# Performance work log

Hardware: AMD Instinct MI355X
Metric: run time of the kernel (lower is better)

Reference implementation:

```python
import jax, jax.numpy as jnp
import numpy as np

NUM_NODES = 50000
NUM_EDGES = 800000
DIM = 96


def setup_inputs() -> dict:
    key = jax.random.key(0)
    k1, k2, k3, k4, k5, k6 = jax.random.split(key, 6)
    x = jax.random.normal(k1, (NUM_NODES, DIM), dtype=jnp.float32)
    edge_index = jax.random.randint(k2, (2, NUM_EDGES), 0, NUM_NODES, dtype=jnp.int64)
    s = 1.0 / np.sqrt(DIM)
    W_self = jax.random.uniform(k3, (DIM, DIM), dtype=jnp.float32, minval=-s, maxval=s)
    b_self = jax.random.uniform(k4, (DIM,), dtype=jnp.float32, minval=-s, maxval=s)
    W_neigh = jax.random.uniform(k5, (DIM, DIM), dtype=jnp.float32, minval=-s, maxval=s)
    b_neigh = jax.random.uniform(k6, (DIM,), dtype=jnp.float32, minval=-s, maxval=s)
    return {"x": x, "edge_index": edge_index, "W_self": W_self, "b_self": b_self,
            "W_neigh": W_neigh, "b_neigh": b_neigh}


def reference(x, edge_index, W_self, b_self, W_neigh, b_neigh):
    source, target = edge_index[0], edge_index[1]
    # scatter-add of gathered source features into target rows
    aggregated = jax.ops.segment_sum(x[source], target, num_segments=NUM_NODES)  # [N, D]
    degree = jax.ops.segment_sum(jnp.ones((NUM_EDGES,), dtype=x.dtype), target,
                                 num_segments=NUM_NODES)[:, None]  # [N, 1]
    neighbor_mean = aggregated / jnp.maximum(degree, 1.0)
    # nn.Linear applies x @ W.T + b
    return x @ W_self.T + b_self + neighbor_mean @ W_neigh.T + b_neigh
```

## Files before the change

### kernel.cpp

```cpp
#include <hip/hip_runtime.h>
#include <hip/hip_bf16.h>

#define N_NODES 50000
#define N_EDGES 800000
#define DIM 96
#define NPART 256
#define PSZ 196
#define NBINBLK 196
#define BINCAP 48
#define BPP (NBINBLK * BINCAP)
#define CAP 4096
#define NPACK_BLOCKS 4688

typedef unsigned int uint;
typedef unsigned short u16;
using u16x8 = __attribute__((ext_vector_type(8))) unsigned short;

__device__ __forceinline__ u16 f2bf(float f) {
    __hip_bfloat16 h = __float2bfloat16(f);
    return *reinterpret_cast<u16*>(&h);
}
__device__ __forceinline__ float bf2f(u16 u) {
    return __uint_as_float(((uint)u) << 16);
}
__device__ __forceinline__ int pdiv(int t) { return (int)(((uint)t * 85599u) >> 24); }

__global__ __launch_bounds__(256) void packbin_k(
    const float* __restrict__ x, const int* __restrict__ ei,
    u16* __restrict__ xbf, uint* __restrict__ part_edges,
    int* __restrict__ counts)
{
    __shared__ uint bins[NPART * BINCAP];
    __shared__ int  bcnt[NPART];
    const int tid = threadIdx.x;

    if (blockIdx.x >= NBINBLK) {
        int pb = blockIdx.x - NBINBLK;
        int i4 = (pb * 256 + tid) * 4;
        if (i4 < N_NODES * DIM) {
            float4 v = *reinterpret_cast<const float4*>(x + i4);
            ushort4 o;
            o.x = f2bf(v.x); o.y = f2bf(v.y); o.z = f2bf(v.z); o.w = f2bf(v.w);
            *reinterpret_cast<ushort4*>(xbf + i4) = o;
        }
        return;
    }

    for (int i = tid; i < NPART; i += 256) bcnt[i] = 0;
    __syncthreads();

    const int e0 = blockIdx.x * 4096 + tid * 16;
    if (e0 + 16 <= N_EDGES) {
#pragma unroll
        for (int j = 0; j < 4; j++) {
            int4 s = *reinterpret_cast<const int4*>(ei + e0 + j * 4);
            int4 t = *reinterpret_cast<const int4*>(ei + N_EDGES + e0 + j * 4);
            int ss[4] = {s.x, s.y, s.z, s.w};
            int tt[4] = {t.x, t.y, t.z, t.w};
#pragma unroll
            for (int k = 0; k < 4; k++) {
                int p = pdiv(tt[k]);
                int local = tt[k] - p * PSZ;
                int slot = atomicAdd(&bcnt[p], 1);
                if (slot < BINCAP)
                    bins[p * BINCAP + slot] = ((uint)local << 16) | (uint)ss[k];
            }
        }
    } else {
        for (int j = 0; j < 16; j++) {
            int e = e0 + j;
            if (e < N_EDGES) {
                int sv = ei[e];
                int tv = ei[N_EDGES + e];
                int p = pdiv(tv);
                int local = tv - p * PSZ;
                int slot = atomicAdd(&bcnt[p], 1);
                if (slot < BINCAP)
                    bins[p * BINCAP + slot] = ((uint)local << 16) | (uint)sv;
            }
        }
    }
    __syncthreads();

    for (int p = tid; p < NPART; p += 256)
        counts[p * NBINBLK + blockIdx.x] = min(bcnt[p], BINCAP);

    for (int i = tid; i < NPART * BINCAP; i += 256) {
        int p = i / BINCAP;
        int s = i - p * BINCAP;
        if (s < bcnt[p])
            part_edges[(size_t)p * BPP + blockIdx.x * BINCAP + s] = bins[i];
    }
}

__device__ __forceinline__ void wave_scan256(int* a, int tid) {
    if (tid < 64) {
        int v0 = a[tid * 4], v1 = a[tid * 4 + 1], v2 = a[tid * 4 + 2], v3 = a[tid * 4 + 3];
        int s01 = v0 + v1;
        int s = s01 + v2 + v3;
        int inc = s;
#pragma unroll
        for (int off = 1; off < 64; off <<= 1) {
            int n = __shfl_up(inc, off, 64);
            if (tid >= off) inc += n;
        }
        int base = inc - s;
        a[tid * 4]     = base + v0;
        a[tid * 4 + 1] = base + s01;
        a[tid * 4 + 2] = base + s01 + v2;
        a[tid * 4 + 3] = base + s;
    }
}

__global__ __launch_bounds__(1024) void fused_k(
    const u16* __restrict__ xbf,
    const uint* __restrict__ part_edges,
    const int* __restrict__ counts,
    const float* __restrict__ Wself, const float* __restrict__ bself,
    const float* __restrict__ Wneigh, const float* __restrict__ bneigh,
    float* __restrict__ out)
{
    using short8 = __attribute__((ext_vector_type(8))) short;
    using f32x4  = __attribute__((ext_vector_type(4))) float;

    __shared__ u16   Axm[208 * 200];
    __shared__ short Bb[96 * 200];
    __shared__ uint  recs[CAP];
    __shared__ u16   ssrc[CAP];
    __shared__ int   bc[256];
    __shared__ int   csc[256];
    __shared__ int   hist[256];
    __shared__ int   cur[256];

    const int tid = threadIdx.x;
    const int p = blockIdx.x;
    const int node0 = p * PSZ;

    for (int idx = tid; idx < 96 * 96; idx += 1024) {
        int j = idx / 96;
        int k = idx - j * 96;
        Bb[j * 200 + k]      = (short)f2bf(Wself[idx]);
        Bb[j * 200 + 96 + k] = (short)f2bf(Wneigh[idx]);
    }

    if (tid < 256) {
        int v = (tid < NBINBLK) ? counts[p * NBINBLK + tid] : 0;
        bc[tid] = v;
        csc[tid] = v;
        cur[tid] = 0;
    }

    for (int i = tid; i < PSZ * 12; i += 1024) {
        int n = i / 12, t = i - n * 12;
        int node = node0 + n;
        short8 v = (short8)0;
        if (node < N_NODES)
            v = *reinterpret_cast<const short8*>(xbf + (size_t)node * DIM + t * 8);
        *reinterpret_cast<short8*>(&Axm[n * 200 + t * 8]) = v;
    }
    __syncthreads();

    wave_scan256(csc, tid);
    __syncthreads();
    int m = csc[255]; if (m > CAP) m = CAP;

    for (int i = tid; i < NBINBLK * BINCAP; i += 1024) {
        int b = i / BINCAP;
        int s = i - b * BINCAP;
        if (s < bc[b]) {
            int dst = csc[b] - bc[b] + s;
            if (dst < CAP)
                recs[dst] = part_edges[(size_t)p * BPP + i];
        }
    }
    __syncthreads();

    for (int i = tid; i < m; i += 1024)
        atomicAdd(&cur[recs[i] >> 16], 1);
    __syncthreads();
    if (tid < 256) hist[tid] = cur[tid];
    __syncthreads();
    wave_scan256(hist, tid);
    __syncthreads();
    if (tid < 256) cur[tid] = hist[tid] - cur[tid];
    __syncthreads();

    for (int i = tid; i < m; i += 1024) {
        uint r = recs[i];
        int pos = atomicAdd(&cur[r >> 16], 1);
        ssrc[pos] = (u16)(r & 0xFFFF);
    }
    __syncthreads();

    if (tid < 1020) {
        const int g = tid / 12;
        const int l = tid - g * 12;
        const int l8 = l * 8;
        for (int r = g; r < PSZ; r += 85) {
            int end = hist[r];
            int beg = (r > 0) ? hist[r - 1] : 0;
            float a0 = 0.f, a1 = 0.f, a2 = 0.f, a3 = 0.f;
            float a4 = 0.f, a5 = 0.f, a6 = 0.f, a7 = 0.f;
            int i = beg;
            for (; i + 3 < end; i += 4) {
                int s0 = ssrc[i], s1 = ssrc[i + 1], s2 = ssrc[i + 2], s3 = ssrc[i + 3];
                u16x8 v0 = *reinterpret_cast<const u16x8*>(xbf + (size_t)s0 * DIM + l8);
                u16x8 v1 = *reinterpret_cast<const u16x8*>(xbf + (size_t)s1 * DIM + l8);
                u16x8 v2 = *reinterpret_cast<const u16x8*>(xbf + (size_t)s2 * DIM + l8);
                u16x8 v3 = *reinterpret_cast<const u16x8*>(xbf + (size_t)s3 * DIM + l8);
                a0 += bf2f(v0[0]) + bf2f(v1[0]) + bf2f(v2[0]) + bf2f(v3[0]);
                a1 += bf2f(v0[1]) + bf2f(v1[1]) + bf2f(v2[1]) + bf2f(v3[1]);
                a2 += bf2f(v0[2]) + bf2f(v1[2]) + bf2f(v2[2]) + bf2f(v3[2]);
                a3 += bf2f(v0[3]) + bf2f(v1[3]) + bf2f(v2[3]) + bf2f(v3[3]);
                a4 += bf2f(v0[4]) + bf2f(v1[4]) + bf2f(v2[4]) + bf2f(v3[4]);
                a5 += bf2f(v0[5]) + bf2f(v1[5]) + bf2f(v2[5]) + bf2f(v3[5]);
                a6 += bf2f(v0[6]) + bf2f(v1[6]) + bf2f(v2[6]) + bf2f(v3[6]);
                a7 += bf2f(v0[7]) + bf2f(v1[7]) + bf2f(v2[7]) + bf2f(v3[7]);
            }
            for (; i < end; i++) {
                int s = ssrc[i];
                u16x8 v = *reinterpret_cast<const u16x8*>(xbf + (size_t)s * DIM + l8);
                a0 += bf2f(v[0]); a1 += bf2f(v[1]); a2 += bf2f(v[2]); a3 += bf2f(v[3]);
                a4 += bf2f(v[4]); a5 += bf2f(v[5]); a6 += bf2f(v[6]); a7 += bf2f(v[7]);
            }
            float inv = (end > beg) ? 1.0f / (float)(end - beg) : 0.f;
            u16x8 o;
            o[0] = f2bf(a0 * inv); o[1] = f2bf(a1 * inv);
            o[2] = f2bf(a2 * inv); o[3] = f2bf(a3 * inv);
            o[4] = f2bf(a4 * inv); o[5] = f2bf(a5 * inv);
            o[6] = f2bf(a6 * inv); o[7] = f2bf(a7 * inv);
            *reinterpret_cast<u16x8*>(&Axm[r * 200 + 96 + l8]) = o;
        }
    }
    __syncthreads();

    const int wave = tid >> 6;
    const int lane = tid & 63;
    const int quad = lane >> 4;
    const int m16  = lane & 15;

    if (wave < 13) {
        const int rloc = wave * 16;
        f32x4 acc[6];
#pragma unroll
        for (int nt = 0; nt < 6; nt++) acc[nt] = (f32x4){0.f, 0.f, 0.f, 0.f};

#pragma unroll
        for (int kt = 0; kt < 6; kt++) {
            short8 a = *reinterpret_cast<const short8*>(
                &Axm[(rloc + m16) * 200 + kt * 32 + quad * 8]);
#pragma unroll
            for (int nt = 0; nt < 6; nt++) {
                short8 b = *reinterpret_cast<const short8*>(
                    &Bb[(nt * 16 + m16) * 200 + kt * 32 + quad * 8]);
                acc[nt] = __builtin_amdgcn_mfma_f32_16x16x32_bf16(a, b, acc[nt], 0, 0, 0);
            }
        }

#pragma unroll
        for (int nt = 0; nt < 6; nt++) {
            int col = nt * 16 + m16;
            float bias = bself[col] + bneigh[col];
#pragma unroll
            for (int reg = 0; reg < 4; reg++) {
                int rl = rloc + quad * 4 + reg;
                int row = node0 + rl;
                if (rl < PSZ && row < N_NODES)
                    out[(size_t)row * DIM + col] = acc[nt][reg] + bias;
            }
        }
    }
}

extern "C" void kernel_launch(void* const* d_in, const int* in_sizes, int n_in,
                              void* d_out, int out_size, void* d_ws, size_t ws_size,
                              hipStream_t stream) {
    const float* x      = (const float*)d_in[0];
    const int*   ei     = (const int*)d_in[1];
    const float* Wself  = (const float*)d_in[2];
    const float* bself  = (const float*)d_in[3];
    const float* Wneigh = (const float*)d_in[4];
    const float* bneigh = (const float*)d_in[5];
    float* out = (float*)d_out;

    uint* part_edges = (uint*)d_ws;
    int*  counts     = (int*)(part_edges + (size_t)NPART * BPP);
    u16*  xbf        = (u16*)(counts + NPART * NBINBLK);

    packbin_k<<<NBINBLK + NPACK_BLOCKS, 256, 0, stream>>>(
        x, ei, xbf, part_edges, counts);
    fused_k<<<NPART, 1024, 0, stream>>>(
        xbf, part_edges, counts, Wself, bself, Wneigh, bneigh, out);
}
```

Before: 123.3 us.

## Merge binning and aggregation kernels into one cooperative kernel with grid sync

Replaces the two-kernel pipeline with one cooperative launch of 256 blocks of 1024 threads. The first 196 blocks bin the edges into shared memory, every block converts a strided slice of x to bf16, and a grid-wide sync then separates this from the gather/MFMA phase. Shared memory is overlaid with a union so both phases fit. This removes a kernel launch boundary but pushes binning and conversion onto only 256 blocks, with each binning thread now handling 4 edges, and adds the cost of a grid barrier.

```diff
diff --git a/kernel.cpp b/kernel.cpp
--- a/kernel.cpp
+++ b/kernel.cpp
@@ -1,5 +1,6 @@
 #include <hip/hip_runtime.h>
 #include <hip/hip_bf16.h>
+#include <hip/hip_cooperative_groups.h>
 
 #define N_NODES 50000
 #define N_EDGES 800000
@@ -10,7 +11,6 @@
 #define BINCAP 48
 #define BPP (NBINBLK * BINCAP)
 #define CAP 4096
-#define NPACK_BLOCKS 4688
 
 typedef unsigned int uint;
 typedef unsigned short u16;
@@ -24,74 +24,6 @@
     return __uint_as_float(((uint)u) << 16);
 }
 __device__ __forceinline__ int pdiv(int t) { return (int)(((uint)t * 85599u) >> 24); }
-
-__global__ __launch_bounds__(256) void packbin_k(
-    const float* __restrict__ x, const int* __restrict__ ei,
-    u16* __restrict__ xbf, uint* __restrict__ part_edges,
-    int* __restrict__ counts)
-{
-    __shared__ uint bins[NPART * BINCAP];
-    __shared__ int  bcnt[NPART];
-    const int tid = threadIdx.x;
-
-    if (blockIdx.x >= NBINBLK) {
-        int pb = blockIdx.x - NBINBLK;
-        int i4 = (pb * 256 + tid) * 4;
-        if (i4 < N_NODES * DIM) {
-            float4 v = *reinterpret_cast<const float4*>(x + i4);
-            ushort4 o;
-            o.x = f2bf(v.x); o.y = f2bf(v.y); o.z = f2bf(v.z); o.w = f2bf(v.w);
-            *reinterpret_cast<ushort4*>(xbf + i4) = o;
-        }
-        return;
-    }
-
-    for (int i = tid; i < NPART; i += 256) bcnt[i] = 0;
-    __syncthreads();
-
-    const int e0 = blockIdx.x * 4096 + tid * 16;
-    if (e0 + 16 <= N_EDGES) {
-#pragma unroll
-        for (int j = 0; j < 4; j++) {
-            int4 s = *reinterpret_cast<const int4*>(ei + e0 + j * 4);
-            int4 t = *reinterpret_cast<const int4*>(ei + N_EDGES + e0 + j * 4);
-            int ss[4] = {s.x, s.y, s.z, s.w};
-            int tt[4] = {t.x, t.y, t.z, t.w};
-#pragma unroll
-            for (int k = 0; k < 4; k++) {
-                int p = pdiv(tt[k]);
-                int local = tt[k] - p * PSZ;
-                int slot = atomicAdd(&bcnt[p], 1);
-                if (slot < BINCAP)
-                    bins[p * BINCAP + slot] = ((uint)local << 16) | (uint)ss[k];
-            }
-        }
-    } else {
-        for (int j = 0; j < 16; j++) {
-            int e = e0 + j;
-            if (e < N_EDGES) {
-                int sv = ei[e];
-                int tv = ei[N_EDGES + e];
-                int p = pdiv(tv);
-                int local = tv - p * PSZ;
-                int slot = atomicAdd(&bcnt[p], 1);
-                if (slot < BINCAP)
-                    bins[p * BINCAP + slot] = ((uint)local << 16) | (uint)sv;
-            }
-        }
-    }
-    __syncthreads();
-
-    for (int p = tid; p < NPART; p += 256)
-        counts[p * NBINBLK + blockIdx.x] = min(bcnt[p], BINCAP);
-
-    for (int i = tid; i < NPART * BINCAP; i += 256) {
-        int p = i / BINCAP;
-        int s = i - p * BINCAP;
-        if (s < bcnt[p])
-            part_edges[(size_t)p * BPP + blockIdx.x * BINCAP + s] = bins[i];
-    }
-}
 
 __device__ __forceinline__ void wave_scan256(int* a, int tid) {
     if (tid < 64) {
@@ -112,10 +44,9 @@
     }
 }
 
-__global__ __launch_bounds__(1024) void fused_k(
-    const u16* __restrict__ xbf,
-    const uint* __restrict__ part_edges,
-    const int* __restrict__ counts,
+__global__ __launch_bounds__(1024) void fused_all(
+    const float* __restrict__ x, const int* __restrict__ ei,
+    u16* __restrict__ xbf, uint* __restrict__ part_edges, int* __restrict__ counts,
     const float* __restrict__ Wself, const float* __restrict__ bself,
     const float* __restrict__ Wneigh, const float* __restrict__ bneigh,
     float* __restrict__ out)
@@ -123,31 +54,98 @@
     using short8 = __attribute__((ext_vector_type(8))) short;
     using f32x4  = __attribute__((ext_vector_type(4))) float;
 
-    __shared__ u16   Axm[208 * 200];
-    __shared__ short Bb[96 * 200];
-    __shared__ uint  recs[CAP];
-    __shared__ u16   ssrc[CAP];
-    __shared__ int   bc[256];
-    __shared__ int   csc[256];
-    __shared__ int   hist[256];
-    __shared__ int   cur[256];
+    __shared__ __align__(16) union {
+        struct {
+            uint bins[NPART * BINCAP];
+            int  bcnt[NPART];
+        } a;
+        struct {
+            u16   Axm[208 * 200];
+            short Bb[96 * 200];
+            uint  recs[CAP];
+            u16   ssrc[CAP];
+            int   bc[256];
+            int   csc[256];
+            int   hist[256];
+            int   cur[256];
+        } b;
+    } sm;
 
     const int tid = threadIdx.x;
     const int p = blockIdx.x;
+
+    if (p < NBINBLK) {
+        if (tid < NPART) sm.a.bcnt[tid] = 0;
+        __syncthreads();
+
+        const int e0 = p * 4096 + tid * 4;
+        if (e0 + 4 <= N_EDGES) {
+            int4 s4 = *reinterpret_cast<const int4*>(ei + e0);
+            int4 t4 = *reinterpret_cast<const int4*>(ei + N_EDGES + e0);
+            int ss[4] = {s4.x, s4.y, s4.z, s4.w};
+            int tt[4] = {t4.x, t4.y, t4.z, t4.w};
+#pragma unroll
+            for (int k = 0; k < 4; k++) {
+                int pp = pdiv(tt[k]);
+                int local = tt[k] - pp * PSZ;
+                int slot = atomicAdd(&sm.a.bcnt[pp], 1);
+                if (slot < BINCAP)
+                    sm.a.bins[pp * BINCAP + slot] = ((uint)local << 16) | (uint)ss[k];
+            }
+        } else {
+            for (int j = 0; j < 4; j++) {
+                int e = e0 + j;
+                if (e < N_EDGES) {
+                    int sv = ei[e];
+                    int tv = ei[N_EDGES + e];
+                    int pp = pdiv(tv);
+                    int local = tv - pp * PSZ;
+                    int slot = atomicAdd(&sm.a.bcnt[pp], 1);
+                    if (slot < BINCAP)
+                        sm.a.bins[pp * BINCAP + slot] = ((uint)local << 16) | (uint)sv;
+                }
+            }
+        }
+        __syncthreads();
+
+        if (tid < NPART)
+            counts[tid * NBINBLK + p] = min(sm.a.bcnt[tid], BINCAP);
+
+        for (int i = tid; i < NPART * BINCAP; i += 1024) {
+            int pc = i / BINCAP;
+            int s = i - pc * BINCAP;
+            if (s < sm.a.bcnt[pc])
+                part_edges[(size_t)pc * BPP + p * BINCAP + s] = sm.a.bins[i];
+        }
+    }
+
+    {
+        const int gid = p * 1024 + tid;
+        for (int i4 = gid; i4 < (N_NODES * DIM) / 4; i4 += NPART * 1024) {
+            float4 v = *reinterpret_cast<const float4*>(x + i4 * 4);
+            ushort4 o;
+            o.x = f2bf(v.x); o.y = f2bf(v.y); o.z = f2bf(v.z); o.w = f2bf(v.w);
+            *reinterpret_cast<ushort4*>(xbf + i4 * 4) = o;
+        }
+    }
+
+    __threadfence();
+    cooperative_groups::this_grid().sync();
+
     const int node0 = p * PSZ;
 
     for (int idx = tid; idx < 96 * 96; idx += 1024) {
         int j = idx / 96;
         int k = idx - j * 96;
-        Bb[j * 200 + k]      = (short)f2bf(Wself[idx]);
-        Bb[j * 200 + 96 + k] = (short)f2bf(Wneigh[idx]);
+        sm.b.Bb[j * 200 + k]      = (short)f2bf(Wself[idx]);
+        sm.b.Bb[j * 200 + 96 + k] = (short)f2bf(Wneigh[idx]);
     }
 
     if (tid < 256) {
         int v = (tid < NBINBLK) ? counts[p * NBINBLK + tid] : 0;
-        bc[tid] = v;
-        csc[tid] = v;
-        cur[tid] = 0;
+        sm.b.bc[tid] = v;
+        sm.b.csc[tid] = v;
+        sm.b.cur[tid] = 0;
     }
 
     for (int i = tid; i < PSZ * 12; i += 1024) {
@@ -156,39 +154,39 @@
         short8 v = (short8)0;
         if (node < N_NODES)
             v = *reinterpret_cast<const short8*>(xbf + (size_t)node * DIM + t * 8);
-        *reinterpret_cast<short8*>(&Axm[n * 200 + t * 8]) = v;
-    }
-    __syncthreads();
-
-    wave_scan256(csc, tid);
-    __syncthreads();
-    int m = csc[255]; if (m > CAP) m = CAP;
+        *reinterpret_cast<short8*>(&sm.b.Axm[n * 200 + t * 8]) = v;
+    }
+    __syncthreads();
+
+    wave_scan256(sm.b.csc, tid);
+    __syncthreads();
+    int m = sm.b.csc[255]; if (m > CAP) m = CAP;
 
     for (int i = tid; i < NBINBLK * BINCAP; i += 1024) {
         int b = i / BINCAP;
         int s = i - b * BINCAP;
-        if (s < bc[b]) {
-            int dst = csc[b] - bc[b] + s;
+        if (s < sm.b.bc[b]) {
+            int dst = sm.b.csc[b] - sm.b.bc[b] + s;
             if (dst < CAP)
-                recs[dst] = part_edges[(size_t)p * BPP + i];
+                sm.b.recs[dst] = part_edges[(size_t)p * BPP + i];
         }
     }
     __syncthreads();
 
     for (int i = tid; i < m; i += 1024)
-        atomicAdd(&cur[recs[i] >> 16], 1);
-    __syncthreads();
-    if (tid < 256) hist[tid] = cur[tid];
-    __syncthreads();
-    wave_scan256(hist, tid);
-    __syncthreads();
-    if (tid < 256) cur[tid] = hist[tid] - cur[tid];
+        atomicAdd(&sm.b.cur[sm.b.recs[i] >> 16], 1);
+    __syncthreads();
+    if (tid < 256) sm.b.hist[tid] = sm.b.cur[tid];
+    __syncthreads();
+    wave_scan256(sm.b.hist, tid);
+    __syncthreads();
+    if (tid < 256) sm.b.cur[tid] = sm.b.hist[tid] - sm.b.cur[tid];
     __syncthreads();
 
     for (int i = tid; i < m; i += 1024) {
-        uint r = recs[i];
-        int pos = atomicAdd(&cur[r >> 16], 1);
-        ssrc[pos] = (u16)(r & 0xFFFF);
+        uint r = sm.b.recs[i];
+        int pos = atomicAdd(&sm.b.cur[r >> 16], 1);
+        sm.b.ssrc[pos] = (u16)(r & 0xFFFF);
     }
     __syncthreads();
 
@@ -197,13 +195,14 @@
         const int l = tid - g * 12;
         const int l8 = l * 8;
         for (int r = g; r < PSZ; r += 85) {
-            int end = hist[r];
-            int beg = (r > 0) ? hist[r - 1] : 0;
+            int end = sm.b.hist[r];
+            int beg = (r > 0) ? sm.b.hist[r - 1] : 0;
             float a0 = 0.f, a1 = 0.f, a2 = 0.f, a3 = 0.f;
             float a4 = 0.f, a5 = 0.f, a6 = 0.f, a7 = 0.f;
             int i = beg;
             for (; i + 3 < end; i += 4) {
-                int s0 = ssrc[i], s1 = ssrc[i + 1], s2 = ssrc[i + 2], s3 = ssrc[i + 3];
+                int s0 = sm.b.ssrc[i], s1 = sm.b.ssrc[i + 1];
+                int s2 = sm.b.ssrc[i + 2], s3 = sm.b.ssrc[i + 3];
                 u16x8 v0 = *reinterpret_cast<const u16x8*>(xbf + (size_t)s0 * DIM + l8);
                 u16x8 v1 = *reinterpret_cast<const u16x8*>(xbf + (size_t)s1 * DIM + l8);
                 u16x8 v2 = *reinterpret_cast<const u16x8*>(xbf + (size_t)s2 * DIM + l8);
@@ -218,7 +217,7 @@
                 a7 += bf2f(v0[7]) + bf2f(v1[7]) + bf2f(v2[7]) + bf2f(v3[7]);
             }
             for (; i < end; i++) {
-                int s = ssrc[i];
+                int s = sm.b.ssrc[i];
                 u16x8 v = *reinterpret_cast<const u16x8*>(xbf + (size_t)s * DIM + l8);
                 a0 += bf2f(v[0]); a1 += bf2f(v[1]); a2 += bf2f(v[2]); a3 += bf2f(v[3]);
                 a4 += bf2f(v[4]); a5 += bf2f(v[5]); a6 += bf2f(v[6]); a7 += bf2f(v[7]);
@@ -229,7 +228,7 @@
             o[2] = f2bf(a2 * inv); o[3] = f2bf(a3 * inv);
             o[4] = f2bf(a4 * inv); o[5] = f2bf(a5 * inv);
             o[6] = f2bf(a6 * inv); o[7] = f2bf(a7 * inv);
-            *reinterpret_cast<u16x8*>(&Axm[r * 200 + 96 + l8]) = o;
+            *reinterpret_cast<u16x8*>(&sm.b.Axm[r * 200 + 96 + l8]) = o;
         }
     }
     __syncthreads();
@@ -248,11 +247,11 @@
 #pragma unroll
         for (int kt = 0; kt < 6; kt++) {
             short8 a = *reinterpret_cast<const short8*>(
-                &Axm[(rloc + m16) * 200 + kt * 32 + quad * 8]);
+                &sm.b.Axm[(rloc + m16) * 200 + kt * 32 + quad * 8]);
 #pragma unroll
             for (int nt = 0; nt < 6; nt++) {
                 short8 b = *reinterpret_cast<const short8*>(
-                    &Bb[(nt * 16 + m16) * 200 + kt * 32 + quad * 8]);
+                    &sm.b.Bb[(nt * 16 + m16) * 200 + kt * 32 + quad * 8]);
                 acc[nt] = __builtin_amdgcn_mfma_f32_16x16x32_bf16(a, b, acc[nt], 0, 0, 0);
             }
         }
@@ -287,8 +286,9 @@
     int*  counts     = (int*)(part_edges + (size_t)NPART * BPP);
     u16*  xbf        = (u16*)(counts + NPART * NBINBLK);
 
-    packbin_k<<<NBINBLK + NPACK_BLOCKS, 256, 0, stream>>>(
-        x, ei, xbf, part_edges, counts);
-    fused_k<<<NPART, 1024, 0, stream>>>(
-        xbf, part_edges, counts, Wself, bself, Wneigh, bneigh, out);
-}
+    void* kargs[] = { (void*)&x, (void*)&ei, (void*)&xbf, (void*)&part_edges,
+                      (void*)&counts, (void*)&Wself, (void*)&bself,
+                      (void*)&Wneigh, (void*)&bneigh, (void*)&out };
+    hipLaunchCooperativeKernel((void*)fused_all, dim3(NPART), dim3(1024),
+                               kargs, 0, stream);
+}
```

New measurement: 263.2 us. 2.13x slower.
